# Kernel optimization log

Measured on AMD Instinct MI355X. Metric: run time of the kernel, lower is better.

The kernel has to match this reference:

```python
import jax, jax.numpy as jnp
import numpy as np

T = 1_000_000          # number of t_eval points (~1 year at 30 s)
N_ROOMS = 10
N = 12                 # 2 latent wall nodes + n_rooms
DT = 30.0              # seconds between t_eval points
LOAD_SCALE = 50.0      # physical_cooling_scaling: W/m^2 scale for sigmoid(loads)


def setup_inputs() -> dict:
    key = jax.random.key(0)
    k1, k2, k3, k4, k5 = jax.random.split(key, 5)
    t_eval = jnp.arange(T, dtype=jnp.float32) * DT
    x0 = 26.0 * jnp.ones((N,), jnp.float32)  # reset_iv: 26 C at every node
    # Stable slow RC dynamics: negative-definite-ish A with small coupling
    A = (-1e-5 * jnp.eye(N, dtype=jnp.float32)
         + 1e-6 * jax.random.normal(k1, (N, N), jnp.float32))
    B = 1e-6 * jax.random.normal(k2, (N, 1 + N_ROOMS), jnp.float32)
    Tout_data = 10.0 + 20.0 * jax.random.uniform(k3, (T,), jnp.float32)  # outdoor temp samples on t_eval grid
    loads_raw = jax.random.normal(k4, (2, N_ROOMS), jnp.float32)         # pre-sigmoid [cool; gain] loads
    room_areas = 10.0 + 40.0 * jax.random.uniform(k5, (N_ROOMS,), jnp.float32)
    return {"t_eval": t_eval, "x0": x0, "A": A, "B": B,
            "Tout_data": Tout_data, "loads_raw": loads_raw, "room_areas": room_areas}


def reference(t_eval, x0, A, B, Tout_data, loads_raw, room_areas):
    # transform + physical scaling of loads (self.transform = sigmoid)
    loads = jax.nn.sigmoid(loads_raw) * LOAD_SCALE
    cool_load, gain_load = loads[0], loads[1]
    action = 0.0  # no cooling policy -> self.action stays 0
    Q_area = -cool_load * action + gain_load            # [n_rooms]
    Q_watts = Q_area * room_areas                        # proportional_heating
    # u = [Tout; Q_watts] so B@u = B[:,0]*Tout + B[:,1:]@Q_watts (Q constant over t)
    b0 = B[:, 0]                                         # [N]
    Bq = B[:, 1:] @ Q_watts                              # [N], constant forcing
    h = t_eval[1] - t_eval[0]                            # uniform step
    # Linear interp of Tout: value at t_i, midpoint t_i+h/2, and t_{i+1}
    To_t = Tout_data[:-1]
    To_n = Tout_data[1:]
    To_m = 0.5 * (To_t + To_n)

    def f(x, To):  # dy/dt = A x + B u
        return A @ x + b0 * To + Bq

    def step(x, tou):
        to_t, to_m, to_n = tou
        k1 = f(x, to_t)
        k2 = f(x + 0.5 * h * k1, to_m)
        k3 = f(x + 0.5 * h * k2, to_m)
        k4 = f(x + h * k3, to_n)
        xn = x + (h / 6.0) * (k1 + 2.0 * k2 + 2.0 * k3 + k4)
        return xn, xn

    _, xs = jax.lax.scan(step, x0, (To_t, To_m, To_n))
    return jnp.concatenate([x0[None, :], xs], axis=0)  # [T, N]
```

## Files before the change

kernel.cpp:

```cpp
#include <hip/hip_runtime.h>
#include <math.h>


#define S_STEPS 999999
#define CH      4
#define BLK     256
#define NB      977
#define NCHUNK  250000
#define LASTFULL 249998

#define OFF_M   0
#define OFF_C   144
#define OFF_AL  156
#define OFF_BE  168
#define OFF_K   192
#define OFF_P2  264
#define OFF_PA  1416
#define OFF_PL  1704
#define OFF_PD  2136
#define OFF_AGG 4440

#define FMA4(Q,a,b,c,d,acc) fmaf((Q).w,(d),fmaf((Q).z,(c),fmaf((Q).y,(b),fmaf((Q).x,(a),(acc)))))

__device__ __forceinline__ void mv_acc(const float* Pf, const float* x, float* y) {
  const float4* P = reinterpret_cast<const float4*>(Pf);
#pragma unroll
  for (int i = 0; i < 12; ++i) {
    float4 a = P[3*i], b = P[3*i+1], c = P[3*i+2];
    y[i] = FMA4(c, x[8],x[9],x[10],x[11],
            FMA4(b, x[4],x[5],x[6],x[7],
             FMA4(a, x[0],x[1],x[2],x[3], y[i])));
  }
}

__device__ __forceinline__ float rowdot(const float* Prow, const float* xv) {
  const float4* P = reinterpret_cast<const float4*>(Prow);
  float4 a = P[0], b = P[1], c = P[2];
  return FMA4(c, xv[8],xv[9],xv[10],xv[11],
          FMA4(b, xv[4],xv[5],xv[6],xv[7],
           FMA4(a, xv[0],xv[1],xv[2],xv[3], 0.f)));
}

__device__ __forceinline__ void fold_chunk(const float* __restrict__ cons,
                                           const float* tos, float* v) {
  const float4* Kq = reinterpret_cast<const float4*>(cons + OFF_K);
  float4 c0=Kq[0], c1=Kq[1], c2=Kq[2];
  v[0]=c0.x; v[1]=c0.y; v[2]=c0.z; v[3]=c0.w;
  v[4]=c1.x; v[5]=c1.y; v[6]=c1.z; v[7]=c1.w;
  v[8]=c2.x; v[9]=c2.y; v[10]=c2.z; v[11]=c2.w;
#pragma unroll
  for (int s = 0; s < 5; ++s) {
    float ts = tos[s];
    float4 ka=Kq[3*(s+1)], kb=Kq[3*(s+1)+1], kc=Kq[3*(s+1)+2];
    v[0]=fmaf(ka.x,ts,v[0]); v[1]=fmaf(ka.y,ts,v[1]); v[2]=fmaf(ka.z,ts,v[2]); v[3]=fmaf(ka.w,ts,v[3]);
    v[4]=fmaf(kb.x,ts,v[4]); v[5]=fmaf(kb.y,ts,v[5]); v[6]=fmaf(kb.z,ts,v[6]); v[7]=fmaf(kb.w,ts,v[7]);
    v[8]=fmaf(kc.x,ts,v[8]); v[9]=fmaf(kc.y,ts,v[9]); v[10]=fmaf(kc.z,ts,v[10]); v[11]=fmaf(kc.w,ts,v[11]);
  }
}

__global__ void __launch_bounds__(512) setup_kernel(
    const float* __restrict__ t_eval, const float* __restrict__ A,
    const float* __restrict__ Bm, const float* __restrict__ loads_raw,
    const float* __restrict__ areas, float* ws) {
  __shared__ double H1[144], H2[144], H3[144], H4[144], Md[144];
  __shared__ double Qa[144], Qb[144];
  __shared__ double C64[144], C128[144], C256[144], C512[144];
  __shared__ double C1024[144], C2048[144], C4096[144];
  __shared__ double cd[12], ald[12], bed[12], b0d[12], bqd[12];
  __shared__ double Vv[3][12], Kd[72];
  int t = threadIdx.x;
  double h = (double)t_eval[1] - (double)t_eval[0];
  if (t < 144) H1[t] = h * (double)A[t];
  if (t < 12) {
    b0d[t] = (double)Bm[t*11];
    double s = 0.0;
    for (int r = 0; r < 10; ++r) {
      double gq = 50.0 / (1.0 + exp(-(double)loads_raw[10 + r]));
      s += (double)Bm[t*11 + 1 + r] * (gq * (double)areas[r]);
    }
    bqd[t] = s;
  }
  if (t < 72) Kd[t] = 0.0;
  __syncthreads();
  if (t < 144) {
    int i=t/12, j=t%12; double s=0.0;
#pragma unroll
    for (int m = 0; m < 12; ++m) s += H1[i*12+m]*H1[m*12+j];
    H2[t]=s;
  }
  __syncthreads();
  if (t < 288) {
    int w=t/144, e=t%144, i=e/12, j=e%12;
    const double* Bp = w ? H2 : H1;
    double s = 0.0;
#pragma unroll
    for (int m = 0; m < 12; ++m) s += H2[i*12+m]*Bp[m*12+j];
    (w ? H4 : H3)[e] = s;
  }
  __syncthreads();
  if (t < 12) {
    double hb=0,h2b=0,h3b=0,hb0=0,h2b0=0,h3b0=0;
#pragma unroll
    for (int m = 0; m < 12; ++m) {
      hb  += H1[t*12+m]*bqd[m]; h2b  += H2[t*12+m]*bqd[m]; h3b  += H3[t*12+m]*bqd[m];
      hb0 += H1[t*12+m]*b0d[m]; h2b0 += H2[t*12+m]*b0d[m]; h3b0 += H3[t*12+m]*b0d[m];
    }
    double h6 = h / 6.0;
    cd[t]  = h6*(6.0*bqd[t] + 3.0*hb + h2b + 0.25*h3b);
    ald[t] = h6*(3.0*b0d[t] + 2.0*hb0 + 0.75*h2b0 + 0.25*h3b0);
    bed[t] = h6*(3.0*b0d[t] + hb0 + 0.25*h2b0);
    Vv[0][t]=ald[t]; Vv[1][t]=bed[t]; Vv[2][t]=cd[t];
    Kd[48+t] += ald[t]; Kd[60+t] += bed[t]; Kd[t] += cd[t];
  }
  if (t >= 144 && t < 288) {
    int e=t-144, i=e/12, j=e%12;
    Md[e] = (i==j ? 1.0 : 0.0) + H1[e] + 0.5*H2[e] + H3[e]/6.0 + H4[e]/24.0;
  }
  __syncthreads();
  if (t < 144) { ws[OFF_M+t] = (float)Md[t]; Qa[t] = Md[t]; }
  if (t < 12) {
    ws[OFF_C+t]=(float)cd[t]; ws[OFF_AL+t]=(float)ald[t]; ws[OFF_BE+t]=(float)bed[t];
  }
  __syncthreads();
  double* src = Qa; double* dst = Qb;
  for (int r = 1; r <= 12; ++r) {
    double acc = 0.0, ks = 0.0;
    if (t < 144) {
      int i=t/12, j=t%12;
#pragma unroll
      for (int m = 0; m < 12; ++m) acc += src[i*12+m]*src[m*12+j];
    }
    int w=0, i2=0;
    if (r <= 3 && t >= 256 && t < 292) {
      w=(t-256)/12; i2=(t-256)%12;
#pragma unroll
      for (int m = 0; m < 12; ++m) ks += Md[i2*12+m]*Vv[w][m];
    }
    __syncthreads();
    if (t < 144) {
      dst[t] = acc;
      if (r >= 2 && r <= 9) ws[OFF_P2+(r-2)*144+t] = (float)acc;
      if (r == 6)  C64[t]=acc;
      if (r == 7)  C128[t]=acc;
      if (r == 8)  C256[t]=acc;
      if (r == 9)  C512[t]=acc;
      if (r == 10) C1024[t]=acc;
      if (r == 11) C2048[t]=acc;
      if (r == 12) C4096[t]=acc;
    }
    if (r <= 3 && t >= 256 && t < 292) {
      Vv[w][i2] = ks;
      if (w == 0) Kd[(4-r)*12+i2] += ks;
      else if (w == 1) Kd[(5-r)*12+i2] += ks;
      else Kd[i2] += ks;
    }
    __syncthreads();
    double* tmp = src; src = dst; dst = tmp;
  }
  if (t < 72) ws[OFF_K+t] = (float)Kd[t];
  if (t < 144) {
    ws[OFF_PL+t]     = (float)C1024[t];
    ws[OFF_PL+144+t] = (float)C2048[t];
    ws[OFF_PD+t]     = (t % 13 == 0) ? 1.f : 0.f;
    ws[OFF_PD+144+t] = (float)C4096[t];
  }
  if (t < 432) {
    int w=t/144, e=t%144, i=e/12, j=e%12;
    const double* Ap = (w==0) ? C64 : ((w==1) ? C256 : C1024);
    const double* Bp = (w==0) ? C128 : ((w==1) ? C512 : C2048);
    double s = 0.0;
#pragma unroll
    for (int m = 0; m < 12; ++m) s += Ap[i*12+m]*Bp[m*12+j];
    if (w==0) ws[OFF_PA+e] = (float)s;
    else if (w==1) ws[OFF_PA+144+e] = (float)s;
    else ws[OFF_PL+2*144+e] = (float)s;
  }
  for (int j = 2; j < 16; ++j) {
    double acc = 0.0;
    if (t < 144) {
      int i=t/12, jj=t%12;
#pragma unroll
      for (int m = 0; m < 12; ++m) acc += src[i*12+m]*C4096[m*12+jj];
    }
    __syncthreads();
    if (t < 144) { dst[t] = acc; ws[OFF_PD+j*144+t] = (float)acc; }
    __syncthreads();
    double* tmp = src; src = dst; dst = tmp;
  }
}

__global__ void __launch_bounds__(BLK, 4) block_agg(
    const float* __restrict__ cons, const float* __restrict__ To,
    const float* __restrict__ x0, float* __restrict__ agg) {
  __shared__ __align__(16) float Tw[48], Ta[24];
  int k = threadIdx.x, b = blockIdx.x;
  int g = b*BLK + k, base = g*CH;
  bool fullc = (g <= LASTFULL);
  float to_[5];
#pragma unroll
  for (int i = 0; i < 5; ++i) to_[i] = 0.f;
  if (fullc) {
    const float4* tp = reinterpret_cast<const float4*>(To + base);
    float4 ta = tp[0];
    to_[0]=ta.x; to_[1]=ta.y; to_[2]=ta.z; to_[3]=ta.w;
    to_[4]=To[base+4];
  }
  float v[12];
  if (fullc) fold_chunk(cons, to_, v);
  else {
#pragma unroll
    for (int i = 0; i < 12; ++i) v[i] = 0.f;
  }
  if (g == 0) {
    float xi[12];
#pragma unroll
    for (int i = 0; i < 12; ++i) xi[i] = x0[i];
    mv_acc(cons + OFF_P2, xi, v);
  }
  int j = k & 63;
#pragma unroll
  for (int l = 0; l < 6; ++l) {
    int off = 1 << l;
    float nb[12];
#pragma unroll
    for (int i = 0; i < 12; ++i) nb[i] = __shfl_up(v[i], (unsigned)off, 64);
    if (j >= off) mv_acc(cons + OFF_P2 + l*144, nb, v);
  }
  if (j == 63) {
#pragma unroll
    for (int i = 0; i < 12; ++i) Tw[(k>>6)*12 + i] = v[i];
  }
  __syncthreads();
  if (k < 24) {
    int p = k/12, comp = k - p*12;
    Ta[k] = rowdot(cons + OFF_P2 + 6*144 + comp*12, Tw + 2*p*12)
          + Tw[(2*p+1)*12 + comp];
  }
  __syncthreads();
  if (k < 12) {
    agg[b*12 + k] = rowdot(cons + OFF_P2 + 7*144 + k*12, Ta) + Ta[12 + k];
  }
}

__global__ void __launch_bounds__(BLK, 2) scan_expand(
    const float* __restrict__ cons, const float* __restrict__ To,
    const float* __restrict__ x0, const float* __restrict__ agg,
    float* __restrict__ out) {
  __shared__ __align__(16) float Tw[48];
  __shared__ __align__(16) float Pw[48];
  __shared__ __align__(16) float lkb[64*12];
  __shared__ __align__(16) float yv[16*12];
  __shared__ __align__(16) float zv[16*12];
  __shared__ __align__(16) float Xs[12];
  __shared__ __align__(16) float Qw[48];
  int k = threadIdx.x, b = blockIdx.x;
  int g = b*BLK + k, base = g*CH;
  bool active = (g < NCHUNK), fullc = (g <= LASTFULL);
  float to_[5];
#pragma unroll
  for (int i = 0; i < 5; ++i) to_[i] = 0.f;
  if (active) {
    const float4* tp = reinterpret_cast<const float4*>(To + base);
    float4 ta = tp[0];
    to_[0]=ta.x; to_[1]=ta.y; to_[2]=ta.z; to_[3]=ta.w;
    to_[4] = fullc ? To[base+4] : 0.f;
  }
  float v[12];
  if (fullc) fold_chunk(cons, to_, v);
  else {
#pragma unroll
    for (int i = 0; i < 12; ++i) v[i] = 0.f;
  }
  if (g == 0) {
    float xi[12];
#pragma unroll
    for (int i = 0; i < 12; ++i) xi[i] = x0[i];
    mv_acc(cons + OFF_P2, xi, v);
  }
  int j = k & 63, w = k >> 6;
#pragma unroll
  for (int l = 0; l < 6; ++l) {
    int off = 1 << l;
    float nb[12];
#pragma unroll
    for (int i = 0; i < 12; ++i) nb[i] = __shfl_up(v[i], (unsigned)off, 64);
    if (j >= off) mv_acc(cons + OFF_P2 + l*144, nb, v);
  }
  float se[12];
#pragma unroll
  for (int i = 0; i < 12; ++i) {
    float u = __shfl_up(v[i], 1u, 64);
    se[i] = (j == 0) ? 0.f : u;
  }
  if (j == 63) {
#pragma unroll
    for (int i = 0; i < 12; ++i) Tw[w*12 + i] = v[i];
  }
#pragma unroll
  for (int r = 0; r < 3; ++r) {
    int idx = k + r*BLK;
    int slot = idx / 12, comp = idx - slot*12;
    int src = b - 1 - slot;
    float acc = 0.f;
    if (src >= 0) {
      int jj = slot & 3;
      const float* ag = agg + src*12;
      acc = (jj == 0) ? ag[comp]
          : rowdot(cons + OFF_PL + (jj-1)*144 + comp*12, ag);
    }
    lkb[idx] = acc;
  }
  __syncthreads();
  if (k < 192) {
    int i = k/12, comp = k - i*12;
    yv[k] = lkb[(4*i)*12+comp] + lkb[(4*i+1)*12+comp]
          + lkb[(4*i+2)*12+comp] + lkb[(4*i+3)*12+comp];
  } else if (k < 216) {
    int q = k - 192;
    if (q < 12) Pw[q] = 0.f;
    else Pw[q] = Tw[q-12];
  }
  __syncthreads();
  if (k < 192) {
    int i = k/12, comp = k - i*12;
    zv[k] = (i == 0) ? yv[comp]
          : rowdot(cons + OFF_PD + i*144 + comp*12, yv + i*12);
  } else if (k < 204) {
    int comp = k - 192;
    Pw[24+comp] = rowdot(cons + OFF_P2 + 6*144 + comp*12, Pw+12) + Tw[12+comp];
  }
  __syncthreads();
  if (k < 12) {
    float s = 0.f;
#pragma unroll
    for (int i = 0; i < 16; ++i) s += zv[i*12 + k];
    Xs[k] = s;
  } else if (k >= 192 && k < 204) {
    int comp = k - 192;
    Pw[36+comp] = rowdot(cons + OFF_P2 + 6*144 + comp*12, Pw+24) + Tw[24+comp];
  }
  __syncthreads();
  if (k < 48) {
    int ww = k/12, comp = k - ww*12;
    float acc;
    if (ww == 0) acc = Xs[comp];
    else if (ww == 1) acc = rowdot(cons + OFF_P2 + 6*144 + comp*12, Xs);
    else if (ww == 2) acc = rowdot(cons + OFF_P2 + 7*144 + comp*12, Xs);
    else acc = rowdot(cons + OFF_PA + 144 + comp*12, Xs);
    Qw[k] = acc + Pw[k];
  }
  __syncthreads();
  if (!active) return;
  float x[12];
#pragma unroll
  for (int i = 0; i < 12; ++i) x[i] = Qw[w*12 + i];
#pragma unroll
  for (int l = 0; l < 6; ++l) {
    if ((j >> l) & 1) {
      float vn[12];
#pragma unroll
      for (int i = 0; i < 12; ++i) vn[i] = 0.f;
      mv_acc(cons + OFF_P2 + l*144, x, vn);
#pragma unroll
      for (int i = 0; i < 12; ++i) x[i] = vn[i];
    }
  }
#pragma unroll
  for (int i = 0; i < 12; ++i) x[i] += se[i];
  if (b == 0 && k == 0) {
#pragma unroll
    for (int i = 0; i < 12; ++i) x[i] += x0[i];
#pragma unroll
    for (int i = 0; i < 12; ++i) out[i] = x0[i];
  }
  float cv[12], av[12], bv[12];
#pragma unroll
  for (int i = 0; i < 12; ++i) {
    cv[i] = cons[OFF_C + i]; av[i] = cons[OFF_AL + i]; bv[i] = cons[OFF_BE + i];
  }
  const float4* Mq = reinterpret_cast<const float4*>(cons + OFF_M);
#pragma unroll
  for (int s = 0; s < CH; ++s) {
    float tot = to_[s], ton = (s < CH-1) ? to_[s+1] : to_[4];
    float xn[12];
#pragma unroll
    for (int i = 0; i < 12; ++i) {
      float4 a = Mq[3*i], bq = Mq[3*i+1], c = Mq[3*i+2];
      xn[i] = FMA4(c, x[8],x[9],x[10],x[11],
               FMA4(bq, x[4],x[5],x[6],x[7],
                FMA4(a, x[0],x[1],x[2],x[3],
                 fmaf(bv[i],ton,fmaf(av[i],tot,cv[i])))));
    }
    int tt = base + s;
    if (tt < S_STEPS) {
      float4* op = reinterpret_cast<float4*>(out + (size_t)(tt+1)*12);
      op[0] = make_float4(xn[0],xn[1],xn[2],xn[3]);
      op[1] = make_float4(xn[4],xn[5],xn[6],xn[7]);
      op[2] = make_float4(xn[8],xn[9],xn[10],xn[11]);
    }
#pragma unroll
    for (int i = 0; i < 12; ++i) x[i] = xn[i];
  }
}

extern "C" void kernel_launch(void* const* d_in, const int* in_sizes, int n_in,
                              void* d_out, int out_size, void* d_ws, size_t ws_size,
                              hipStream_t stream) {
  const float* t_eval    = (const float*)d_in[0];
  const float* x0        = (const float*)d_in[1];
  const float* A         = (const float*)d_in[2];
  const float* B         = (const float*)d_in[3];
  const float* To        = (const float*)d_in[4];
  const float* loads_raw = (const float*)d_in[5];
  const float* areas     = (const float*)d_in[6];
  float* out = (float*)d_out;
  float* ws  = (float*)d_ws;

  setup_kernel<<<1, 512, 0, stream>>>(t_eval, A, B, loads_raw, areas, ws);
  block_agg<<<NB, BLK, 0, stream>>>(ws, To, x0, ws + OFF_AGG);
  scan_expand<<<NB, BLK, 0, stream>>>(ws, To, x0, ws + OFF_AGG, out);
}
```

Measured before the change: 133.6 us.

## Double per-thread chunk length to 8 steps, halving blocks and scan depth

Each thread now folds and replays 8 RK4 steps instead of 4, so the scan covers half as many chunks and launches half as many blocks. The precomputed matrix powers, forcing kernels and cross-block lookback tables in the setup kernel are rebuilt to match the larger stride (M^8 based powers and a shorter lookback window). In exchange each thread does a longer serial replay and holds more registers, and launch bounds are relaxed to 2 blocks per SM.

```diff
diff --git a/kernel.cpp b/kernel.cpp
--- a/kernel.cpp
+++ b/kernel.cpp
@@ -3,22 +3,22 @@
 
 
 #define S_STEPS 999999
-#define CH      4
+#define CH      8
 #define BLK     256
-#define NB      977
-#define NCHUNK  250000
-#define LASTFULL 249998
+#define NB      489
+#define NCHUNK  125000
+#define LASTFULL 124998
 
 #define OFF_M   0
 #define OFF_C   144
 #define OFF_AL  156
 #define OFF_BE  168
 #define OFF_K   192
-#define OFF_P2  264
-#define OFF_PA  1416
-#define OFF_PL  1704
-#define OFF_PD  2136
-#define OFF_AGG 4440
+#define OFF_P2  320
+#define OFF_PA  1472
+#define OFF_PL  1616
+#define OFF_PD  2048
+#define OFF_AGG 3200
 
 #define FMA4(Q,a,b,c,d,acc) fmaf((Q).w,(d),fmaf((Q).z,(c),fmaf((Q).y,(b),fmaf((Q).x,(a),(acc)))))
 
@@ -49,7 +49,7 @@
   v[4]=c1.x; v[5]=c1.y; v[6]=c1.z; v[7]=c1.w;
   v[8]=c2.x; v[9]=c2.y; v[10]=c2.z; v[11]=c2.w;
 #pragma unroll
-  for (int s = 0; s < 5; ++s) {
+  for (int s = 0; s < 9; ++s) {
     float ts = tos[s];
     float4 ka=Kq[3*(s+1)], kb=Kq[3*(s+1)+1], kc=Kq[3*(s+1)+2];
     v[0]=fmaf(ka.x,ts,v[0]); v[1]=fmaf(ka.y,ts,v[1]); v[2]=fmaf(ka.z,ts,v[2]); v[3]=fmaf(ka.w,ts,v[3]);
@@ -64,10 +64,10 @@
     const float* __restrict__ areas, float* ws) {
   __shared__ double H1[144], H2[144], H3[144], H4[144], Md[144];
   __shared__ double Qa[144], Qb[144];
-  __shared__ double C64[144], C128[144], C256[144], C512[144];
-  __shared__ double C1024[144], C2048[144], C4096[144];
+  __shared__ double C512s[144], C1024s[144], C2048s[144], C4096s[144];
+  __shared__ double C8192s[144], C16384s[144], C32768s[144], Pd3s[144];
   __shared__ double cd[12], ald[12], bed[12], b0d[12], bqd[12];
-  __shared__ double Vv[3][12], Kd[72];
+  __shared__ double Vv[3][12], Kd[120];
   int t = threadIdx.x;
   double h = (double)t_eval[1] - (double)t_eval[0];
   if (t < 144) H1[t] = h * (double)A[t];
@@ -80,7 +80,7 @@
     }
     bqd[t] = s;
   }
-  if (t < 72) Kd[t] = 0.0;
+  if (t < 120) Kd[t] = 0.0;
   __syncthreads();
   if (t < 144) {
     int i=t/12, j=t%12; double s=0.0;
@@ -110,7 +110,7 @@
     ald[t] = h6*(3.0*b0d[t] + 2.0*hb0 + 0.75*h2b0 + 0.25*h3b0);
     bed[t] = h6*(3.0*b0d[t] + hb0 + 0.25*h2b0);
     Vv[0][t]=ald[t]; Vv[1][t]=bed[t]; Vv[2][t]=cd[t];
-    Kd[48+t] += ald[t]; Kd[60+t] += bed[t]; Kd[t] += cd[t];
+    Kd[96+t] += ald[t]; Kd[108+t] += bed[t]; Kd[t] += cd[t];
   }
   if (t >= 144 && t < 288) {
     int e=t-144, i=e/12, j=e%12;
@@ -123,7 +123,7 @@
   }
   __syncthreads();
   double* src = Qa; double* dst = Qb;
-  for (int r = 1; r <= 12; ++r) {
+  for (int r = 1; r <= 15; ++r) {
     double acc = 0.0, ks = 0.0;
     if (t < 144) {
       int i=t/12, j=t%12;
@@ -131,7 +131,7 @@
       for (int m = 0; m < 12; ++m) acc += src[i*12+m]*src[m*12+j];
     }
     int w=0, i2=0;
-    if (r <= 3 && t >= 256 && t < 292) {
+    if (r <= 7 && t >= 256 && t < 292) {
       w=(t-256)/12; i2=(t-256)%12;
 #pragma unroll
       for (int m = 0; m < 12; ++m) ks += Md[i2*12+m]*Vv[w][m];
@@ -139,71 +139,64 @@
     __syncthreads();
     if (t < 144) {
       dst[t] = acc;
-      if (r >= 2 && r <= 9) ws[OFF_P2+(r-2)*144+t] = (float)acc;
-      if (r == 6)  C64[t]=acc;
-      if (r == 7)  C128[t]=acc;
-      if (r == 8)  C256[t]=acc;
-      if (r == 9)  C512[t]=acc;
-      if (r == 10) C1024[t]=acc;
-      if (r == 11) C2048[t]=acc;
-      if (r == 12) C4096[t]=acc;
-    }
-    if (r <= 3 && t >= 256 && t < 292) {
+      if (r >= 3 && r <= 10) ws[OFF_P2+(r-3)*144+t] = (float)acc;
+      if (r == 9)  C512s[t]=acc;
+      if (r == 10) C1024s[t]=acc;
+      if (r == 11) { C2048s[t]=acc;  ws[OFF_PL+t]       = (float)acc; }
+      if (r == 12) { C4096s[t]=acc;  ws[OFF_PL+144+t]   = (float)acc; }
+      if (r == 13) { C8192s[t]=acc;  ws[OFF_PD+144+t]   = (float)acc; }
+      if (r == 14) { C16384s[t]=acc; ws[OFF_PD+2*144+t] = (float)acc; }
+      if (r == 15) { C32768s[t]=acc; ws[OFF_PD+4*144+t] = (float)acc; }
+    }
+    if (r <= 7 && t >= 256 && t < 292) {
       Vv[w][i2] = ks;
-      if (w == 0) Kd[(4-r)*12+i2] += ks;
-      else if (w == 1) Kd[(5-r)*12+i2] += ks;
+      if (w == 0) Kd[(8-r)*12+i2] += ks;
+      else if (w == 1) Kd[(9-r)*12+i2] += ks;
       else Kd[i2] += ks;
     }
     __syncthreads();
     double* tmp = src; src = dst; dst = tmp;
   }
-  if (t < 72) ws[OFF_K+t] = (float)Kd[t];
-  if (t < 144) {
-    ws[OFF_PL+t]     = (float)C1024[t];
-    ws[OFF_PL+144+t] = (float)C2048[t];
-    ws[OFF_PD+t]     = (t % 13 == 0) ? 1.f : 0.f;
-    ws[OFF_PD+144+t] = (float)C4096[t];
-  }
+  if (t < 120) ws[OFF_K+t] = (float)Kd[t];
+  if (t < 144) ws[OFF_PD+t] = (t % 13 == 0) ? 1.f : 0.f;
   if (t < 432) {
     int w=t/144, e=t%144, i=e/12, j=e%12;
-    const double* Ap = (w==0) ? C64 : ((w==1) ? C256 : C1024);
-    const double* Bp = (w==0) ? C128 : ((w==1) ? C512 : C2048);
+    const double* Ap = (w==0) ? C512s  : ((w==1) ? C2048s : C8192s);
+    const double* Bp = (w==0) ? C1024s : ((w==1) ? C4096s : C16384s);
     double s = 0.0;
 #pragma unroll
     for (int m = 0; m < 12; ++m) s += Ap[i*12+m]*Bp[m*12+j];
     if (w==0) ws[OFF_PA+e] = (float)s;
-    else if (w==1) ws[OFF_PA+144+e] = (float)s;
-    else ws[OFF_PL+2*144+e] = (float)s;
-  }
-  for (int j = 2; j < 16; ++j) {
-    double acc = 0.0;
-    if (t < 144) {
-      int i=t/12, jj=t%12;
-#pragma unroll
-      for (int m = 0; m < 12; ++m) acc += src[i*12+m]*C4096[m*12+jj];
-    }
-    __syncthreads();
-    if (t < 144) { dst[t] = acc; ws[OFF_PD+j*144+t] = (float)acc; }
-    __syncthreads();
-    double* tmp = src; src = dst; dst = tmp;
-  }
-}
-
-__global__ void __launch_bounds__(BLK, 4) block_agg(
+    else if (w==1) ws[OFF_PL+2*144+e] = (float)s;
+    else { ws[OFF_PD+3*144+e] = (float)s; Pd3s[e] = s; }
+  }
+  __syncthreads();
+  if (t < 432) {
+    int w=t/144, e=t%144, i=e/12, j=e%12;
+    const double* Ap = (w==0) ? C8192s : ((w==1) ? C16384s : Pd3s);
+    double s = 0.0;
+#pragma unroll
+    for (int m = 0; m < 12; ++m) s += Ap[i*12+m]*C32768s[m*12+j];
+    ws[OFF_PD+(5+w)*144+e] = (float)s;
+  }
+}
+
+__global__ void __launch_bounds__(BLK, 2) block_agg(
     const float* __restrict__ cons, const float* __restrict__ To,
     const float* __restrict__ x0, float* __restrict__ agg) {
   __shared__ __align__(16) float Tw[48], Ta[24];
   int k = threadIdx.x, b = blockIdx.x;
   int g = b*BLK + k, base = g*CH;
   bool fullc = (g <= LASTFULL);
-  float to_[5];
-#pragma unroll
-  for (int i = 0; i < 5; ++i) to_[i] = 0.f;
+  float to_[9];
+#pragma unroll
+  for (int i = 0; i < 9; ++i) to_[i] = 0.f;
   if (fullc) {
     const float4* tp = reinterpret_cast<const float4*>(To + base);
-    float4 ta = tp[0];
+    float4 ta = tp[0], tb = tp[1];
     to_[0]=ta.x; to_[1]=ta.y; to_[2]=ta.z; to_[3]=ta.w;
-    to_[4]=To[base+4];
+    to_[4]=tb.x; to_[5]=tb.y; to_[6]=tb.z; to_[7]=tb.w;
+    to_[8]=To[base+8];
   }
   float v[12];
   if (fullc) fold_chunk(cons, to_, v);
@@ -248,22 +241,23 @@
     float* __restrict__ out) {
   __shared__ __align__(16) float Tw[48];
   __shared__ __align__(16) float Pw[48];
-  __shared__ __align__(16) float lkb[64*12];
-  __shared__ __align__(16) float yv[16*12];
-  __shared__ __align__(16) float zv[16*12];
+  __shared__ __align__(16) float lkb[32*12];
+  __shared__ __align__(16) float yv[8*12];
+  __shared__ __align__(16) float zv[8*12];
   __shared__ __align__(16) float Xs[12];
   __shared__ __align__(16) float Qw[48];
   int k = threadIdx.x, b = blockIdx.x;
   int g = b*BLK + k, base = g*CH;
   bool active = (g < NCHUNK), fullc = (g <= LASTFULL);
-  float to_[5];
-#pragma unroll
-  for (int i = 0; i < 5; ++i) to_[i] = 0.f;
+  float to_[9];
+#pragma unroll
+  for (int i = 0; i < 9; ++i) to_[i] = 0.f;
   if (active) {
     const float4* tp = reinterpret_cast<const float4*>(To + base);
-    float4 ta = tp[0];
+    float4 ta = tp[0], tb = tp[1];
     to_[0]=ta.x; to_[1]=ta.y; to_[2]=ta.z; to_[3]=ta.w;
-    to_[4] = fullc ? To[base+4] : 0.f;
+    to_[4]=tb.x; to_[5]=tb.y; to_[6]=tb.z; to_[7]=tb.w;
+    to_[8] = fullc ? To[base+8] : 0.f;
   }
   float v[12];
   if (fullc) fold_chunk(cons, to_, v);
@@ -297,35 +291,37 @@
     for (int i = 0; i < 12; ++i) Tw[w*12 + i] = v[i];
   }
 #pragma unroll
-  for (int r = 0; r < 3; ++r) {
+  for (int r = 0; r < 2; ++r) {
     int idx = k + r*BLK;
-    int slot = idx / 12, comp = idx - slot*12;
-    int src = b - 1 - slot;
-    float acc = 0.f;
-    if (src >= 0) {
-      int jj = slot & 3;
-      const float* ag = agg + src*12;
-      acc = (jj == 0) ? ag[comp]
-          : rowdot(cons + OFF_PL + (jj-1)*144 + comp*12, ag);
-    }
-    lkb[idx] = acc;
-  }
-  __syncthreads();
-  if (k < 192) {
+    if (idx < 384) {
+      int slot = idx / 12, comp = idx - slot*12;
+      int src = b - 1 - slot;
+      float acc = 0.f;
+      if (src >= 0) {
+        int jj = slot & 3;
+        const float* ag = agg + src*12;
+        acc = (jj == 0) ? ag[comp]
+            : rowdot(cons + OFF_PL + (jj-1)*144 + comp*12, ag);
+      }
+      lkb[idx] = acc;
+    }
+  }
+  __syncthreads();
+  if (k < 96) {
     int i = k/12, comp = k - i*12;
     yv[k] = lkb[(4*i)*12+comp] + lkb[(4*i+1)*12+comp]
           + lkb[(4*i+2)*12+comp] + lkb[(4*i+3)*12+comp];
-  } else if (k < 216) {
+  } else if (k >= 192 && k < 216) {
     int q = k - 192;
     if (q < 12) Pw[q] = 0.f;
     else Pw[q] = Tw[q-12];
   }
   __syncthreads();
-  if (k < 192) {
+  if (k < 96) {
     int i = k/12, comp = k - i*12;
     zv[k] = (i == 0) ? yv[comp]
           : rowdot(cons + OFF_PD + i*144 + comp*12, yv + i*12);
-  } else if (k < 204) {
+  } else if (k >= 192 && k < 204) {
     int comp = k - 192;
     Pw[24+comp] = rowdot(cons + OFF_P2 + 6*144 + comp*12, Pw+12) + Tw[12+comp];
   }
@@ -333,7 +329,7 @@
   if (k < 12) {
     float s = 0.f;
 #pragma unroll
-    for (int i = 0; i < 16; ++i) s += zv[i*12 + k];
+    for (int i = 0; i < 8; ++i) s += zv[i*12 + k];
     Xs[k] = s;
   } else if (k >= 192 && k < 204) {
     int comp = k - 192;
@@ -346,7 +342,7 @@
     if (ww == 0) acc = Xs[comp];
     else if (ww == 1) acc = rowdot(cons + OFF_P2 + 6*144 + comp*12, Xs);
     else if (ww == 2) acc = rowdot(cons + OFF_P2 + 7*144 + comp*12, Xs);
-    else acc = rowdot(cons + OFF_PA + 144 + comp*12, Xs);
+    else acc = rowdot(cons + OFF_PA + comp*12, Xs);
     Qw[k] = acc + Pw[k];
   }
   __syncthreads();
@@ -381,7 +377,7 @@
   const float4* Mq = reinterpret_cast<const float4*>(cons + OFF_M);
 #pragma unroll
   for (int s = 0; s < CH; ++s) {
-    float tot = to_[s], ton = (s < CH-1) ? to_[s+1] : to_[4];
+    float tot = to_[s], ton = to_[s+1];
     float xn[12];
 #pragma unroll
     for (int i = 0; i < 12; ++i) {
```

After: 132.5 us. No clear change (-0.9%).
